# Performance work log

Hardware: AMD Instinct MI355X
Metric: run time of the kernel (lower is better)

The kernel has to match this reference:

```python
import jax, jax.numpy as jnp
import numpy as np

B, S, D_IN, D_HID, D_OUT = 32, 512, 768, 3072, 768


def setup_inputs() -> dict:
    key = jax.random.key(0)
    k1, k2, k3, k4 = jax.random.split(key, 4)
    init_k = float(np.sqrt(1.0 / D_IN))
    init_k2 = float(np.sqrt(1.0 / D_HID))
    x = jax.random.normal(k1, (B, S, D_IN), dtype=jnp.float32)
    in_weight = jax.random.uniform(k2, (D_HID, D_IN), dtype=jnp.float32, minval=-init_k, maxval=init_k)
    in_bias = jax.random.uniform(k3, (D_HID,), dtype=jnp.float32, minval=-init_k, maxval=init_k)
    out_weight = jax.random.uniform(k4, (D_HID, D_OUT), dtype=jnp.float32, minval=-init_k2, maxval=init_k2)
    return {"x": x, "in_weight": in_weight, "in_bias": in_bias, "out_weight": out_weight}


def reference(x, in_weight, in_bias, out_weight):
    # flatten leading dims to tokens: [B*S, D_IN]
    lead = x.shape[:-1]
    xt = x.reshape(-1, in_weight.shape[1])
    # hidden = GELU(x @ W_in^T + b)   (in_weight stored [hidden, in])
    h = jax.nn.gelu(jnp.einsum('td,hd->th', xt, in_weight) + in_bias, approximate=False)
    # out = hidden @ W_out            (out_weight stored [hidden, out]; no output bias)
    out = jnp.einsum('th,ho->to', h, out_weight)
    return out.reshape(*lead, out_weight.shape[1])
```

## Files before the change

kernel.cpp:

```cpp
#include <hip/hip_runtime.h>

typedef short bf16x8 __attribute__((ext_vector_type(8)));
typedef float f32x4  __attribute__((ext_vector_type(4)));

__device__ __forceinline__ unsigned short f2bf(float f) {
    unsigned int u = __float_as_uint(f);
    u += 0x7FFFu + ((u >> 16) & 1u);
    return (unsigned short)(u >> 16);
}

__device__ __forceinline__ float gelu_f(float x) {
    float x2 = x * x;
    float u = x * (-1.5957691216f - 0.0713548162f * x2);
    float e = __expf(u);
    return x * __builtin_amdgcn_rcpf(1.0f + e);
}

__global__ void cvt_f32_bf16(const float* __restrict__ in,
                             unsigned short* __restrict__ out, int n4) {
    int stride = gridDim.x * blockDim.x;
    for (int i = blockIdx.x * blockDim.x + threadIdx.x; i < n4; i += stride) {
        float4 v = ((const float4*)in)[i];
        ushort4 r;
        r.x = f2bf(v.x); r.y = f2bf(v.y); r.z = f2bf(v.z); r.w = f2bf(v.w);
        ((ushort4*)out)[i] = r;
    }
}

__global__ void transpose_cvt(const float* __restrict__ in,
                              unsigned short* __restrict__ out, int H, int O) {
    __shared__ float tile[32][33];
    int o0 = blockIdx.x * 32, h0 = blockIdx.y * 32;
    int tx = threadIdx.x, ty = threadIdx.y;
    #pragma unroll
    for (int r = 0; r < 32; r += 8)
        tile[ty + r][tx] = in[(size_t)(h0 + ty + r) * O + o0 + tx];
    __syncthreads();
    #pragma unroll
    for (int r = 0; r < 32; r += 8) {
        int o = ty + r;
        out[(size_t)(o0 + o) * H + h0 + tx] = f2bf(tile[tx][o]);
    }
}

template <int EPI, int K, int N, int BN>
__global__ __launch_bounds__(512, 2) void gemm_8ph(
    const unsigned short* __restrict__ A,
    const unsigned short* __restrict__ B,
    const float* __restrict__ bias,
    void* __restrict__ Cp) {
    constexpr int NREP = BN / 64;
    __shared__ __align__(16) char lds[131072];
    const int t = threadIdx.x;
    const int w = t >> 6, l = t & 63;
    constexpr int ntiles = N / BN;

    int bid = blockIdx.x, nwg = gridDim.x;
    int wgid = ((nwg & 7) == 0) ? ((bid & 7) * (nwg >> 3) + (bid >> 3)) : bid;
    const int mt = wgid / ntiles, nt = wgid % ntiles;
    const int m0 = mt << 8, n0 = nt * BN;
    const int wr = w >> 2, wc = w & 3;

    const int u1 = t + 512;
    const int gu0 = (t >> 2) * K + (((t & 3) ^ ((t >> 3) & 3)) << 3);
    const int gu1 = (u1 >> 2) * K + (((u1 & 3) ^ ((u1 >> 3) & 3)) << 3);
    const unsigned short* Abase = A + (size_t)m0 * K;
    const unsigned short* Bbase = B + (size_t)n0 * K;

#define STAGE(PTR, KT, KS, REG) { \
    const unsigned short* g_ = (PTR) + (KT) * 64 + (KS) * 32; \
    __builtin_amdgcn_global_load_lds( \
        (const __attribute__((address_space(1))) void*)(g_ + gu0), \
        (__attribute__((address_space(3))) void*)(lds + (REG) + t * 16), 16, 0, 0); \
    __builtin_amdgcn_global_load_lds( \
        (const __attribute__((address_space(1))) void*)(g_ + gu1), \
        (__attribute__((address_space(3))) void*)(lds + (REG) + 8192 + t * 16), 16, 0, 0); }
#define PIN() { __builtin_amdgcn_sched_barrier(0); asm volatile("" ::: "memory"); }
#define GATE() { asm volatile("s_waitcnt vmcnt(8)\n\ts_barrier" ::: "memory"); \
                 __builtin_amdgcn_sched_barrier(0); }
#define LGKM() { __builtin_amdgcn_sched_barrier(0); \
                 asm volatile("s_waitcnt lgkmcnt(0)" ::: "memory"); \
                 __builtin_amdgcn_sched_barrier(0); }
#define RDB(RG) { const char* p_ = lds + (RG) + boffb; \
    _Pragma("unroll") \
    for (int ni_ = 0; ni_ < NREP; ++ni_) bv[ni_] = *(const bf16x8*)(p_ + ni_ * 1024); }
#define RDA(RG, MH) { const char* p_ = lds + (RG) + aoffb + (MH) * 4096; \
    av[0] = *(const bf16x8*)(p_);        av[1] = *(const bf16x8*)(p_ + 1024); \
    av[2] = *(const bf16x8*)(p_ + 2048); av[3] = *(const bf16x8*)(p_ + 3072); }
#define MFMAQ(MB) \
    _Pragma("unroll") \
    for (int mi = 0; mi < 4; ++mi) { \
        _Pragma("unroll") \
        for (int ni = 0; ni < NREP; ++ni) \
            acc[MB * 4 + mi][ni] = __builtin_amdgcn_mfma_f32_16x16x32_bf16( \
                av[mi], bv[ni], acc[MB * 4 + mi][ni], 0, 0, 0); \
    } \
    __builtin_amdgcn_s_setprio(0); \
    __builtin_amdgcn_sched_barrier(0);

    const int cR = l >> 4, lr = l & 15;
    const int swz = (cR ^ ((lr >> 1) & 3)) << 4;
    const int aoffb = (wr * 128 + lr) * 64 + swz;
    const int boffb = 32768 + (wc * (BN / 4) + lr) * 64 + swz;

    f32x4 acc[8][NREP];
    {
        f32x4 z = {0.f, 0.f, 0.f, 0.f};
        #pragma unroll
        for (int i = 0; i < 8; ++i)
            #pragma unroll
            for (int j = 0; j < NREP; ++j) acc[i][j] = z;
    }
    bf16x8 av[4], bv[NREP];

    constexpr int NTK = K >> 6;
    constexpr int NT2 = K >> 7;

    STAGE(Abase, 0, 0, 0);             PIN();
    STAGE(Bbase, 0, 0, 32768);         PIN();
    STAGE(Abase, 0, 1, 16384);         PIN();
    STAGE(Bbase, 0, 1, 49152);         PIN();
    STAGE(Abase, 1, 0, 65536);         PIN();
    STAGE(Bbase, 1, 0, 98304);         PIN();

    for (int tt = 0; tt < NT2; ++tt) {
        const int k1 = (2 * tt + 1 < NTK) ? 2 * tt + 1 : NTK - 1;
        const int k2 = (2 * tt + 2 < NTK) ? 2 * tt + 2 : NTK - 1;
        const int k3 = (2 * tt + 3 < NTK) ? 2 * tt + 3 : NTK - 1;
        GATE(); RDB(0); RDA(0, 0);
        STAGE(Abase, k1, 1, 81920);
        LGKM(); __builtin_amdgcn_s_setprio(1); MFMAQ(0);
        RDA(0, 1);
        STAGE(Bbase, k1, 1, 114688);
        LGKM(); __builtin_amdgcn_s_setprio(1); MFMAQ(1);
        GATE(); RDB(16384); RDA(16384, 0);
        STAGE(Abase, k2, 0, 0);
        LGKM(); __builtin_amdgcn_s_setprio(1); MFMAQ(0);
        RDA(16384, 1);
        STAGE(Bbase, k2, 0, 32768);
        LGKM(); __builtin_amdgcn_s_setprio(1); MFMAQ(1);
        GATE(); RDB(65536); RDA(65536, 0);
        STAGE(Abase, k2, 1, 16384);
        LGKM(); __builtin_amdgcn_s_setprio(1); MFMAQ(0);
        RDA(65536, 1);
        STAGE(Bbase, k2, 1, 49152);
        LGKM(); __builtin_amdgcn_s_setprio(1); MFMAQ(1);
        GATE(); RDB(81920); RDA(81920, 0);
        STAGE(Abase, k3, 0, 65536);
        LGKM(); __builtin_amdgcn_s_setprio(1); MFMAQ(0);
        RDA(81920, 1);
        STAGE(Bbase, k3, 0, 98304);
        LGKM(); __builtin_amdgcn_s_setprio(1); MFMAQ(1);
    }
#undef STAGE
#undef PIN
#undef GATE
#undef LGKM
#undef RDB
#undef RDA
#undef MFMAQ

    const int colb = n0 + wc * (BN / 4) + lr;
    if constexpr (EPI == 0) {
        unsigned short* Cb = (unsigned short*)Cp;
        float bvs[NREP];
        #pragma unroll
        for (int ni = 0; ni < NREP; ++ni) bvs[ni] = bias[colb + ni * 16];
        #pragma unroll
        for (int mi = 0; mi < 8; ++mi)
            #pragma unroll
            for (int j = 0; j < 4; ++j) {
                size_t row = m0 + wr * 128 + mi * 16 + cR * 4 + j;
                #pragma unroll
                for (int ni = 0; ni < NREP; ++ni) {
                    float v = acc[mi][ni][j] + bvs[ni];
                    Cb[row * N + colb + ni * 16] = f2bf(gelu_f(v));
                }
            }
    } else {
        float* Cf = (float*)Cp;
        #pragma unroll
        for (int mi = 0; mi < 8; ++mi)
            #pragma unroll
            for (int j = 0; j < 4; ++j) {
                size_t row = m0 + wr * 128 + mi * 16 + cR * 4 + j;
                #pragma unroll
                for (int ni = 0; ni < NREP; ++ni)
                    Cf[row * N + colb + ni * 16] = acc[mi][ni][j];
            }
    }
}

extern "C" void kernel_launch(void* const* d_in, const int* in_sizes, int n_in,
                              void* d_out, int out_size, void* d_ws, size_t ws_size,
                              hipStream_t stream) {
    const float* x  = (const float*)d_in[0];
    const float* w1 = (const float*)d_in[1];
    const float* b1 = (const float*)d_in[2];
    const float* w2 = (const float*)d_in[3];
    float* out = (float*)d_out;

    const int T = 16384, DIN = 768, DH = 3072, DOUT = 768;

    unsigned short* xb  = (unsigned short*)d_ws;
    unsigned short* w1b = xb  + (size_t)T * DIN;
    unsigned short* w2t = w1b + (size_t)DH * DIN;
    unsigned short* h   = w2t + (size_t)DOUT * DH;

    size_t fixed = ((size_t)T * DIN + (size_t)DH * DIN + (size_t)DOUT * DH) * 2;
    int CH = T;
    while (CH > 256 && fixed + (size_t)CH * DH * 2 > ws_size) CH >>= 1;

    cvt_f32_bf16<<<2048, 256, 0, stream>>>(x, xb, T * DIN / 4);
    cvt_f32_bf16<<<1024, 256, 0, stream>>>(w1, w1b, DH * DIN / 4);
    transpose_cvt<<<dim3(DOUT / 32, DH / 32), dim3(32, 8), 0, stream>>>(w2, w2t, DH, DOUT);

    for (int c0 = 0; c0 < T; c0 += CH) {
        gemm_8ph<0, 768, 3072, 256><<<(CH / 256) * (DH / 256), 512, 0, stream>>>(
            xb + (size_t)c0 * DIN, w1b, b1, h);
        gemm_8ph<1, 3072, 768, 192><<<(CH / 256) * (DOUT / 192), 512, 0, stream>>>(
            h, w2t, b1, out + (size_t)c0 * DOUT);
    }
}
```

Baseline: 188.0 us.

## Restructure GEMM pipeline sync with per-phase barriers and half-tile vmcnt waits

Replaces the per-k-tile combined vmcnt(8)+barrier gate with a schedule that puts barriers around every MFMA phase and waits on global loads (vmcnt(4)) only once per two k-subtiles. Priority raising moves into the MFMA macro. The aim is to lock waves into a ping-pong rhythm where LDS reads and global-to-LDS staging overlap MFMA work, and to cut how often the pipeline stalls on outstanding loads. In exchange it adds many more s_barrier instructions per iteration, which could serialize waves and add overhead. The new load waits also depend on exact ordering of the outstanding loads to stay correct.

```diff
diff --git a/kernel.cpp b/kernel.cpp
--- a/kernel.cpp
+++ b/kernel.cpp
@@ -76,10 +76,11 @@
         (const __attribute__((address_space(1))) void*)(g_ + gu1), \
         (__attribute__((address_space(3))) void*)(lds + (REG) + 8192 + t * 16), 16, 0, 0); }
 #define PIN() { __builtin_amdgcn_sched_barrier(0); asm volatile("" ::: "memory"); }
-#define GATE() { asm volatile("s_waitcnt vmcnt(8)\n\ts_barrier" ::: "memory"); \
+#define BARR() { asm volatile("s_barrier" ::: "memory"); \
                  __builtin_amdgcn_sched_barrier(0); }
-#define LGKM() { __builtin_amdgcn_sched_barrier(0); \
-                 asm volatile("s_waitcnt lgkmcnt(0)" ::: "memory"); \
+#define VMC4() { asm volatile("s_waitcnt vmcnt(4)" ::: "memory"); \
+                 __builtin_amdgcn_sched_barrier(0); }
+#define LGKM() { asm volatile("s_waitcnt lgkmcnt(0)" ::: "memory"); \
                  __builtin_amdgcn_sched_barrier(0); }
 #define RDB(RG) { const char* p_ = lds + (RG) + boffb; \
     _Pragma("unroll") \
@@ -88,6 +89,7 @@
     av[0] = *(const bf16x8*)(p_);        av[1] = *(const bf16x8*)(p_ + 1024); \
     av[2] = *(const bf16x8*)(p_ + 2048); av[3] = *(const bf16x8*)(p_ + 3072); }
 #define MFMAQ(MB) \
+    __builtin_amdgcn_s_setprio(1); \
     _Pragma("unroll") \
     for (int mi = 0; mi < 4; ++mi) { \
         _Pragma("unroll") \
@@ -122,39 +124,42 @@
     STAGE(Bbase, 0, 1, 49152);         PIN();
     STAGE(Abase, 1, 0, 65536);         PIN();
     STAGE(Bbase, 1, 0, 98304);         PIN();
+    VMC4(); BARR();
 
     for (int tt = 0; tt < NT2; ++tt) {
-        const int k1 = (2 * tt + 1 < NTK) ? 2 * tt + 1 : NTK - 1;
+        const int k1 = 2 * tt + 1;
         const int k2 = (2 * tt + 2 < NTK) ? 2 * tt + 2 : NTK - 1;
         const int k3 = (2 * tt + 3 < NTK) ? 2 * tt + 3 : NTK - 1;
-        GATE(); RDB(0); RDA(0, 0);
-        STAGE(Abase, k1, 1, 81920);
-        LGKM(); __builtin_amdgcn_s_setprio(1); MFMAQ(0);
-        RDA(0, 1);
-        STAGE(Bbase, k1, 1, 114688);
-        LGKM(); __builtin_amdgcn_s_setprio(1); MFMAQ(1);
-        GATE(); RDB(16384); RDA(16384, 0);
-        STAGE(Abase, k2, 0, 0);
-        LGKM(); __builtin_amdgcn_s_setprio(1); MFMAQ(0);
-        RDA(16384, 1);
-        STAGE(Bbase, k2, 0, 32768);
-        LGKM(); __builtin_amdgcn_s_setprio(1); MFMAQ(1);
-        GATE(); RDB(65536); RDA(65536, 0);
-        STAGE(Abase, k2, 1, 16384);
-        LGKM(); __builtin_amdgcn_s_setprio(1); MFMAQ(0);
-        RDA(65536, 1);
-        STAGE(Bbase, k2, 1, 49152);
-        LGKM(); __builtin_amdgcn_s_setprio(1); MFMAQ(1);
-        GATE(); RDB(81920); RDA(81920, 0);
-        STAGE(Abase, k3, 0, 65536);
-        LGKM(); __builtin_amdgcn_s_setprio(1); MFMAQ(0);
-        RDA(81920, 1);
-        STAGE(Bbase, k3, 0, 98304);
-        LGKM(); __builtin_amdgcn_s_setprio(1); MFMAQ(1);
-    }
+        RDB(0); RDA(0, 0); PIN();
+        STAGE(Abase, k1, 1, 81920); PIN();
+        BARR(); LGKM(); MFMAQ(0); BARR();
+        RDA(0, 1); PIN();
+        STAGE(Bbase, k1, 1, 114688); PIN();
+        BARR(); LGKM(); MFMAQ(1); BARR();
+        RDB(16384); RDA(16384, 0); PIN();
+        STAGE(Abase, k2, 0, 0); PIN();
+        BARR(); LGKM(); MFMAQ(0); BARR();
+        RDA(16384, 1); PIN();
+        STAGE(Bbase, k2, 0, 32768); PIN();
+        VMC4(); BARR(); LGKM(); MFMAQ(1); BARR();
+        RDB(65536); RDA(65536, 0); PIN();
+        STAGE(Abase, k2, 1, 16384); PIN();
+        BARR(); LGKM(); MFMAQ(0); BARR();
+        RDA(65536, 1); PIN();
+        STAGE(Bbase, k2, 1, 49152); PIN();
+        BARR(); LGKM(); MFMAQ(1); BARR();
+        RDB(81920); RDA(81920, 0); PIN();
+        STAGE(Abase, k3, 0, 65536); PIN();
+        BARR(); LGKM(); MFMAQ(0); BARR();
+        RDA(81920, 1); PIN();
+        STAGE(Bbase, k3, 0, 98304); PIN();
+        VMC4(); BARR(); LGKM(); MFMAQ(1); BARR();
+    }
+    asm volatile("s_waitcnt vmcnt(0)" ::: "memory");
 #undef STAGE
 #undef PIN
-#undef GATE
+#undef BARR
+#undef VMC4
 #undef LGKM
 #undef RDB
 #undef RDA
```

Measured after the change: 190.4 us. No clear change (+1.3%).

## Merge prep kernels and restructure GEMM phases to load full A before MFMA

Applied to the files above, without the earlier changes.

Fuses the three conversion/transpose prep kernels into a single launch that transposes W2 tiles and then grid-strides over x and W1 conversion. In the GEMM main loop, each phase now reads both A halves into separate registers up front, issues both A and B global-to-LDS stages, waits once on LDS reads, then runs both MFMA quarters back to back, instead of interleaving a second LDS read and stage between them. This removes one lgkm wait per phase and two launch overheads, at the cost of extra VGPRs for the second A fragment set and less overlap of the second stage with compute. A final vmcnt(0) drain is added after the loop.

```diff
diff --git a/kernel.cpp b/kernel.cpp
--- a/kernel.cpp
+++ b/kernel.cpp
@@ -16,35 +16,37 @@
     return x * __builtin_amdgcn_rcpf(1.0f + e);
 }
 
-__global__ void cvt_f32_bf16(const float* __restrict__ in,
-                             unsigned short* __restrict__ out, int n4) {
-    int stride = gridDim.x * blockDim.x;
-    for (int i = blockIdx.x * blockDim.x + threadIdx.x; i < n4; i += stride) {
-        float4 v = ((const float4*)in)[i];
-        ushort4 r;
-        r.x = f2bf(v.x); r.y = f2bf(v.y); r.z = f2bf(v.z); r.w = f2bf(v.w);
-        ((ushort4*)out)[i] = r;
-    }
-}
-
-__global__ void transpose_cvt(const float* __restrict__ in,
-                              unsigned short* __restrict__ out, int H, int O) {
+__global__ void prep_all(const float* __restrict__ x,
+                         const float* __restrict__ w1,
+                         const float* __restrict__ w2,
+                         unsigned short* __restrict__ xb,
+                         unsigned short* __restrict__ w1b,
+                         unsigned short* __restrict__ w2t) {
     __shared__ float tile[32][33];
-    int o0 = blockIdx.x * 32, h0 = blockIdx.y * 32;
-    int tx = threadIdx.x, ty = threadIdx.y;
+    const int b = blockIdx.x, t = threadIdx.x;
+    const int tx = t & 31, ty = t >> 5;
+    const int o0 = (b % 24) * 32, h0 = (b / 24) * 32;
     #pragma unroll
     for (int r = 0; r < 32; r += 8)
-        tile[ty + r][tx] = in[(size_t)(h0 + ty + r) * O + o0 + tx];
+        tile[ty + r][tx] = w2[(size_t)(h0 + ty + r) * 768 + o0 + tx];
     __syncthreads();
     #pragma unroll
     for (int r = 0; r < 32; r += 8) {
         int o = ty + r;
-        out[(size_t)(o0 + o) * H + h0 + tx] = f2bf(tile[tx][o]);
+        w2t[(size_t)(o0 + o) * 3072 + h0 + tx] = f2bf(tile[tx][o]);
+    }
+    constexpr int NX = 16384 * 768 / 4, NW = 3072 * 768 / 4;
+    const int stride = gridDim.x * 256;
+    for (int i = b * 256 + t; i < NX + NW; i += stride) {
+        const float4 v = (i < NX) ? ((const float4*)x)[i] : ((const float4*)w1)[i - NX];
+        ushort4 r;
+        r.x = f2bf(v.x); r.y = f2bf(v.y); r.z = f2bf(v.z); r.w = f2bf(v.w);
+        if (i < NX) ((ushort4*)xb)[i] = r; else ((ushort4*)w1b)[i - NX] = r;
     }
 }
 
 template <int EPI, int K, int N, int BN>
-__global__ __launch_bounds__(512, 2) void gemm_8ph(
+__global__ __launch_bounds__(512, 2) void gemm_m4(
     const unsigned short* __restrict__ A,
     const unsigned short* __restrict__ B,
     const float* __restrict__ bias,
@@ -84,19 +86,25 @@
 #define RDB(RG) { const char* p_ = lds + (RG) + boffb; \
     _Pragma("unroll") \
     for (int ni_ = 0; ni_ < NREP; ++ni_) bv[ni_] = *(const bf16x8*)(p_ + ni_ * 1024); }
-#define RDA(RG, MH) { const char* p_ = lds + (RG) + aoffb + (MH) * 4096; \
-    av[0] = *(const bf16x8*)(p_);        av[1] = *(const bf16x8*)(p_ + 1024); \
-    av[2] = *(const bf16x8*)(p_ + 2048); av[3] = *(const bf16x8*)(p_ + 3072); }
-#define MFMAQ(MB) \
+#define RDA(RG, MH, DST) { const char* p_ = lds + (RG) + aoffb + (MH) * 4096; \
+    DST[0] = *(const bf16x8*)(p_);        DST[1] = *(const bf16x8*)(p_ + 1024); \
+    DST[2] = *(const bf16x8*)(p_ + 2048); DST[3] = *(const bf16x8*)(p_ + 3072); }
+#define MFMAQ(MB, AV) \
+    __builtin_amdgcn_s_setprio(1); \
     _Pragma("unroll") \
     for (int mi = 0; mi < 4; ++mi) { \
         _Pragma("unroll") \
         for (int ni = 0; ni < NREP; ++ni) \
             acc[MB * 4 + mi][ni] = __builtin_amdgcn_mfma_f32_16x16x32_bf16( \
-                av[mi], bv[ni], acc[MB * 4 + mi][ni], 0, 0, 0); \
+                AV[mi], bv[ni], acc[MB * 4 + mi][ni], 0, 0, 0); \
     } \
     __builtin_amdgcn_s_setprio(0); \
     __builtin_amdgcn_sched_barrier(0);
+#define PHASE(RG, SK, SS, RA, SKB, SSB) { \
+    GATE(); RDB(RG); RDA(RG, 0, av); RDA(RG, 1, avh); PIN(); \
+    STAGE(Abase, SK, SS, RA); PIN(); \
+    STAGE(Bbase, SKB, SSB, (RA) + 32768); PIN(); \
+    LGKM(); MFMAQ(0, av); MFMAQ(1, avh); }
 
     const int cR = l >> 4, lr = l & 15;
     const int swz = (cR ^ ((lr >> 1) & 3)) << 4;
@@ -111,7 +119,7 @@
             #pragma unroll
             for (int j = 0; j < NREP; ++j) acc[i][j] = z;
     }
-    bf16x8 av[4], bv[NREP];
+    bf16x8 av[4], avh[4], bv[NREP];
 
     constexpr int NTK = K >> 6;
     constexpr int NT2 = K >> 7;
@@ -124,34 +132,15 @@
     STAGE(Bbase, 1, 0, 98304);         PIN();
 
     for (int tt = 0; tt < NT2; ++tt) {
-        const int k1 = (2 * tt + 1 < NTK) ? 2 * tt + 1 : NTK - 1;
+        const int k1 = 2 * tt + 1;
         const int k2 = (2 * tt + 2 < NTK) ? 2 * tt + 2 : NTK - 1;
         const int k3 = (2 * tt + 3 < NTK) ? 2 * tt + 3 : NTK - 1;
-        GATE(); RDB(0); RDA(0, 0);
-        STAGE(Abase, k1, 1, 81920);
-        LGKM(); __builtin_amdgcn_s_setprio(1); MFMAQ(0);
-        RDA(0, 1);
-        STAGE(Bbase, k1, 1, 114688);
-        LGKM(); __builtin_amdgcn_s_setprio(1); MFMAQ(1);
-        GATE(); RDB(16384); RDA(16384, 0);
-        STAGE(Abase, k2, 0, 0);
-        LGKM(); __builtin_amdgcn_s_setprio(1); MFMAQ(0);
-        RDA(16384, 1);
-        STAGE(Bbase, k2, 0, 32768);
-        LGKM(); __builtin_amdgcn_s_setprio(1); MFMAQ(1);
-        GATE(); RDB(65536); RDA(65536, 0);
-        STAGE(Abase, k2, 1, 16384);
-        LGKM(); __builtin_amdgcn_s_setprio(1); MFMAQ(0);
-        RDA(65536, 1);
-        STAGE(Bbase, k2, 1, 49152);
-        LGKM(); __builtin_amdgcn_s_setprio(1); MFMAQ(1);
-        GATE(); RDB(81920); RDA(81920, 0);
-        STAGE(Abase, k3, 0, 65536);
-        LGKM(); __builtin_amdgcn_s_setprio(1); MFMAQ(0);
-        RDA(81920, 1);
-        STAGE(Bbase, k3, 0, 98304);
-        LGKM(); __builtin_amdgcn_s_setprio(1); MFMAQ(1);
-    }
+        PHASE(0,     k1, 1, 81920, k1, 1);
+        PHASE(16384, k2, 0, 0,     k2, 0);
+        PHASE(65536, k2, 1, 16384, k2, 1);
+        PHASE(81920, k3, 0, 65536, k3, 0);
+    }
+    asm volatile("s_waitcnt vmcnt(0)" ::: "memory");
 #undef STAGE
 #undef PIN
 #undef GATE
@@ -159,6 +148,7 @@
 #undef RDB
 #undef RDA
 #undef MFMAQ
+#undef PHASE
 
     const int colb = n0 + wc * (BN / 4) + lr;
     if constexpr (EPI == 0) {
@@ -211,14 +201,12 @@
     int CH = T;
     while (CH > 256 && fixed + (size_t)CH * DH * 2 > ws_size) CH >>= 1;
 
-    cvt_f32_bf16<<<2048, 256, 0, stream>>>(x, xb, T * DIN / 4);
-    cvt_f32_bf16<<<1024, 256, 0, stream>>>(w1, w1b, DH * DIN / 4);
-    transpose_cvt<<<dim3(DOUT / 32, DH / 32), dim3(32, 8), 0, stream>>>(w2, w2t, DH, DOUT);
+    prep_all<<<2304, 256, 0, stream>>>(x, w1, w2, xb, w1b, w2t);
 
     for (int c0 = 0; c0 < T; c0 += CH) {
-        gemm_8ph<0, 768, 3072, 256><<<(CH / 256) * (DH / 256), 512, 0, stream>>>(
+        gemm_m4<0, 768, 3072, 256><<<(CH / 256) * (DH / 256), 512, 0, stream>>>(
             xb + (size_t)c0 * DIN, w1b, b1, h);
-        gemm_8ph<1, 3072, 768, 192><<<(CH / 256) * (DOUT / 192), 512, 0, stream>>>(
+        gemm_m4<1, 3072, 768, 192><<<(CH / 256) * (DOUT / 192), 512, 0, stream>>>(
             h, w2t, b1, out + (size_t)c0 * DOUT);
     }
 }
```

New measurement: 187.1 us (median of 2 runs). About the same (-0.5%).
